# Kernel tuning notes

Measured on AMD Instinct MI355X. Metric: run time of the kernel, lower is better.

The kernel has to match this reference:

```python
import jax, jax.numpy as jnp
import numpy as np

B, S, D, H = 2, 1024, 768, 12
HD = D // H          # head_dim = 64
DFF = 4 * D          # 3072
EPS = 1e-5


def _ln(x, g, b):
    m = x.mean(-1, keepdims=True)
    v = ((x - m) ** 2).mean(-1, keepdims=True)
    return (x - m) * jax.lax.rsqrt(v + EPS) * g + b


def setup_inputs() -> dict:
    key = jax.random.key(0)
    ks = jax.random.split(key, 8)
    w = lambda k, shape: jax.random.normal(k, shape, jnp.float32) * 0.02
    return {
        "inp": jax.random.normal(ks[0], (B, S, D), jnp.float32),
        "attention_mask": jnp.zeros((B, S), bool),  # True = masked out (filled with -inf)
        "rel_matrix": jax.random.randint(ks[1], (B, S, S), -1, 2, jnp.int32),  # values in {-1,0,1}
        "qkv_w": w(ks[2], (3 * D, D)),
        "rel_A": w(ks[3], (3, HD)),        # relative_position_emb_A.weight
        "o_w": w(ks[4], (D, D)),
        "w1": w(ks[5], (DFF, D)), "b1": jnp.zeros((DFF,), jnp.float32),
        "w2": w(ks[6], (D, DFF)), "b2": jnp.zeros((D,), jnp.float32),
        "ln1_g": jnp.ones((D,), jnp.float32), "ln1_b": jnp.zeros((D,), jnp.float32),
        "ln2_g": jnp.ones((D,), jnp.float32), "ln2_b": jnp.zeros((D,), jnp.float32),
    }


def reference(inp, attention_mask, rel_matrix, qkv_w, rel_A, o_w,
              w1, b1, w2, b2, ln1_g, ln1_b, ln2_g, ln2_b):
    x = _ln(inp, ln1_g, ln1_b)
    qkv = x @ qkv_w.T                                  # (B,S,3D)
    q, k, v = jnp.split(qkv, 3, axis=-1)
    heads = lambda t: t.reshape(B, S, H, HD).transpose(0, 2, 1, 3)  # (B,H,S,HD)
    q, k, v = heads(q), heads(k), heads(v)

    # q @ (k + rel_emb)^T without materializing k_aug:
    # q.k^T term plus per-(q,key) relative term gathered from q @ A^T.
    logits = jnp.einsum("bhqd,bhkd->bhqk", q, k)       # (B,H,S,S)
    r = jnp.einsum("bhqd,cd->bhqc", q, rel_A)          # (B,H,S,3)
    idx = (rel_matrix + 1).astype(jnp.int32)           # (B,S,S) in {0,1,2}
    rel = jnp.take_along_axis(r, jnp.broadcast_to(idx[:, None], (B, H, S, S)), axis=-1)
    logits = (logits + rel) / np.sqrt(HD).astype(np.float32)
    # masked_fill: -inf where mask is True
    logits = jnp.where(attention_mask[:, None, None, :], -jnp.inf, logits)

    attn = jax.nn.softmax(logits, axis=-1)
    out = jnp.einsum("bhqk,bhkd->bhqd", attn, v)
    out = out.transpose(0, 2, 1, 3).reshape(B, S, D)
    inp = inp + out @ o_w.T                            # residual (dropout=0)

    h = _ln(inp, ln2_g, ln2_b)
    mlp = jax.nn.relu(h @ w1.T + b1) @ w2.T + b2
    return inp + mlp
```

## Files before the change

kernel.cpp:

```cpp
#include <hip/hip_runtime.h>
#include <hip/hip_bf16.h>

#define BB 2
#define SS 1024
#define DD 768
#define HH 12
#define HD 64
#define DFF 3072
#define EPS 1e-5f
#define BS2 (BB * SS)
#define BSD ((size_t)BS2 * DD)

typedef unsigned short ushort_t;
typedef unsigned char uchar_t;
using short8 = __attribute__((ext_vector_type(8))) short;
using f32x4  = __attribute__((ext_vector_type(4))) float;

__device__ __forceinline__ ushort_t f2bf_rne(float f) {
    union { float f; unsigned u; } x; x.f = f;
    unsigned r = x.u + 0x7fff + ((x.u >> 16) & 1);
    return (ushort_t)(r >> 16);
}
__device__ __forceinline__ float bf2f(short u) {
    union { unsigned i; float f; } x;
    x.i = ((unsigned)(ushort_t)u) << 16;
    return x.f;
}

#define CVT_N1 (3 * DD * DD / 4)
#define CVT_N2 (CVT_N1 + DD * DD / 4)
#define CVT_N3 (CVT_N2 + DFF * DD / 4)
#define CVT_NT (CVT_N3 + DD * DFF / 4)

__global__ __launch_bounds__(256) void cvt_all(
    const float* __restrict__ qkv_w, const float* __restrict__ o_w,
    const float* __restrict__ w1, const float* __restrict__ w2,
    ushort_t* __restrict__ dst)
{
    int i = blockIdx.x * 256 + threadIdx.x;
    if (i >= CVT_NT) return;
    const float* src; int off;
    if (i < CVT_N1)      { src = qkv_w; off = i; }
    else if (i < CVT_N2) { src = o_w;   off = i - CVT_N1; }
    else if (i < CVT_N3) { src = w1;    off = i - CVT_N2; }
    else                 { src = w2;    off = i - CVT_N3; }
    float4 v = ((const float4*)src)[off];
    ushort4 o;
    o.x = f2bf_rne(v.x); o.y = f2bf_rne(v.y);
    o.z = f2bf_rne(v.z); o.w = f2bf_rne(v.w);
    ((ushort4*)dst)[i] = o;
}

__global__ __launch_bounds__(256) void build_codes(
    const int* __restrict__ rel, const uchar_t* __restrict__ mask,
    unsigned* __restrict__ codes)
{
    int tid = blockIdx.x * 256 + threadIdx.x;
    int l15 = tid & 15;
    int kt  = (tid >> 4) & 15;
    int q   = (tid >> 8) & (SS - 1);
    int b   = tid >> 18;
    const int* rrow = rel + ((size_t)(b * SS + q)) * SS + kt * 64 + l15;
    const uchar_t* mrow = mask + (size_t)b * SS + kt * 64 + l15;
    unsigned o = 0;
#pragma unroll
    for (int nt = 0; nt < 4; ++nt) {
        unsigned c = mrow[nt * 16] ? 3u : (unsigned)(rrow[nt * 16] + 1);
        o |= c << (8 * nt);
    }
    codes[((size_t)(b * SS + q) * 16 + kt) * 16 + l15] = o;
}

__global__ __launch_bounds__(256) void ln_kernel_bf(
    const float* __restrict__ x, const float* __restrict__ g,
    const float* __restrict__ b, ushort_t* __restrict__ y)
{
    const int row = blockIdx.x;
    const float* xr = x + (size_t)row * DD;
    float s = 0.f, ss = 0.f;
    for (int i = threadIdx.x; i < DD; i += 256) {
        float v = xr[i];
        s += v; ss += v * v;
    }
    for (int off = 32; off; off >>= 1) {
        s  += __shfl_down(s,  off);
        ss += __shfl_down(ss, off);
    }
    __shared__ float reds[4], redss[4], bc[2];
    int t = threadIdx.x;
    if ((t & 63) == 0) { reds[t >> 6] = s; redss[t >> 6] = ss; }
    __syncthreads();
    if (t == 0) {
        float S1 = reds[0] + reds[1] + reds[2] + reds[3];
        float S2 = redss[0] + redss[1] + redss[2] + redss[3];
        float mean = S1 / DD;
        float var = S2 / DD - mean * mean;
        bc[0] = mean;
        bc[1] = rsqrtf(var + EPS);
    }
    __syncthreads();
    float mean = bc[0], inv = bc[1];
    ushort_t* yr = y + (size_t)row * DD;
    for (int i = threadIdx.x; i < DD; i += 256) {
        yr[i] = f2bf_rne((xr[i] - mean) * inv * g[i] + b[i]);
    }
}

__global__ __launch_bounds__(256) void merge2_ln_kernel(
    const float* __restrict__ part, const float* __restrict__ inp,
    const float* __restrict__ g, const float* __restrict__ b,
    float* __restrict__ resid, ushort_t* __restrict__ h_bf)
{
    const int row = blockIdx.x;
    const int t = threadIdx.x;
    float4 v = make_float4(0.f, 0.f, 0.f, 0.f);
    const size_t idx = (size_t)row * (DD / 4) + t;
    if (t < DD / 4) {
        v = ((const float4*)inp)[idx];
        float4 p0 = ((const float4*)part)[idx];
        float4 p1 = ((const float4*)(part + BSD))[idx];
        v.x += p0.x + p1.x; v.y += p0.y + p1.y;
        v.z += p0.z + p1.z; v.w += p0.w + p1.w;
        ((float4*)resid)[idx] = v;
    }
    float s  = v.x + v.y + v.z + v.w;
    float ss = v.x * v.x + v.y * v.y + v.z * v.z + v.w * v.w;
    for (int off = 32; off; off >>= 1) {
        s  += __shfl_down(s,  off);
        ss += __shfl_down(ss, off);
    }
    __shared__ float reds[4], redss[4], bc[2];
    if ((t & 63) == 0) { reds[t >> 6] = s; redss[t >> 6] = ss; }
    __syncthreads();
    if (t == 0) {
        float S1 = reds[0] + reds[1] + reds[2] + reds[3];
        float S2 = redss[0] + redss[1] + redss[2] + redss[3];
        float mean = S1 / DD;
        float var = S2 / DD - mean * mean;
        bc[0] = mean;
        bc[1] = rsqrtf(var + EPS);
    }
    __syncthreads();
    if (t < DD / 4) {
        const float mean = bc[0], inv = bc[1];
        float4 gv = ((const float4*)g)[t];
        float4 bv = ((const float4*)b)[t];
        ushort4 o;
        o.x = f2bf_rne((v.x - mean) * inv * gv.x + bv.x);
        o.y = f2bf_rne((v.y - mean) * inv * gv.y + bv.y);
        o.z = f2bf_rne((v.z - mean) * inv * gv.z + bv.z);
        o.w = f2bf_rne((v.w - mean) * inv * gv.w + bv.w);
        ((ushort4*)h_bf)[idx] = o;
    }
}

__global__ __launch_bounds__(256) void merge4_kernel(
    const float* __restrict__ part, const float* __restrict__ resid,
    const float* __restrict__ b2, float* __restrict__ outp, int n4)
{
    int i = blockIdx.x * 256 + threadIdx.x;
    if (i >= n4) return;
    float4 v = ((const float4*)resid)[i];
    int col4 = (i * 4) % DD;
    float4 bv = *(const float4*)(b2 + col4);
    v.x += bv.x; v.y += bv.y; v.z += bv.z; v.w += bv.w;
#pragma unroll
    for (int z = 0; z < 4; ++z) {
        float4 pz = ((const float4*)(part + (size_t)z * BSD))[i];
        v.x += pz.x; v.y += pz.y; v.z += pz.z; v.w += pz.w;
    }
    ((float4*)outp)[i] = v;
}

template <bool RELU, bool OUT_BF16, bool HAS_BIAS, bool PARTIAL>
__global__ __launch_bounds__(256) void gemm_tile(
    const ushort_t* __restrict__ A, const ushort_t* __restrict__ W,
    const float* __restrict__ bias, void* __restrict__ Cout,
    int M, int N, int K, int Ksplit)
{
    __shared__ __align__(16) ushort_t As[1024 * 8];
    __shared__ __align__(16) ushort_t Bs[512 * 8];

    const int t  = threadIdx.x;
    const int n0 = blockIdx.x * 64;
    const int m0 = blockIdx.y * 128;
    const int kb = blockIdx.z * Ksplit;
    const int w  = t >> 6;
    const int l  = t & 63;
    const int wm = (w & 1) * 64;
    const int wn = (w >> 1) * 32;
    const int l15  = l & 15;
    const int quad = l >> 4;

    const ushort_t* gA = A + (size_t)(m0 + (t & 127)) * K + kb + (t >> 7) * 8;
    ushort_t* lA = &As[(size_t)t * 8];
    const ushort_t* gB = W + (size_t)(n0 + (t & 63)) * K + kb + (t >> 6) * 8;
    ushort_t* lB = &Bs[(size_t)t * 8];

    f32x4 acc[4][2] = {};

    for (int k0 = 0; k0 < Ksplit; k0 += 64) {
        __syncthreads();
#pragma unroll
        for (int ii = 0; ii < 4; ++ii)
            __builtin_amdgcn_global_load_lds(
                (const __attribute__((address_space(1))) unsigned int*)(gA + k0 + ii * 16),
                (__attribute__((address_space(3))) unsigned int*)(lA + (size_t)ii * 256 * 8),
                16, 0, 0);
#pragma unroll
        for (int ii = 0; ii < 2; ++ii)
            __builtin_amdgcn_global_load_lds(
                (const __attribute__((address_space(1))) unsigned int*)(gB + k0 + ii * 32),
                (__attribute__((address_space(3))) unsigned int*)(lB + (size_t)ii * 256 * 8),
                16, 0, 0);
        __syncthreads();

#pragma unroll
        for (int ks = 0; ks < 2; ++ks) {
            const ushort_t* aptr = &As[(size_t)((ks * 4 + quad) * 128 + wm + l15) * 8];
            const ushort_t* bptr = &Bs[(size_t)((ks * 4 + quad) * 64 + wn + l15) * 8];
            short8 af[4], bf[2];
#pragma unroll
            for (int i = 0; i < 4; ++i)
                af[i] = *(const short8*)(aptr + (size_t)i * 16 * 8);
#pragma unroll
            for (int j = 0; j < 2; ++j)
                bf[j] = *(const short8*)(bptr + (size_t)j * 16 * 8);
#pragma unroll
            for (int i = 0; i < 4; ++i)
#pragma unroll
                for (int j = 0; j < 2; ++j)
                    acc[i][j] = __builtin_amdgcn_mfma_f32_16x16x32_bf16(
                        af[i], bf[j], acc[i][j], 0, 0, 0);
        }
    }

    if (PARTIAL) {
        float* Cp = (float*)Cout + (size_t)blockIdx.z * ((size_t)M * N);
#pragma unroll
        for (int i = 0; i < 4; ++i) {
            const int row = m0 + wm + i * 16 + quad * 4;
#pragma unroll
            for (int j = 0; j < 2; ++j) {
                const int col = n0 + wn + j * 16 + l15;
#pragma unroll
                for (int r = 0; r < 4; ++r)
                    Cp[(size_t)(row + r) * N + col] = acc[i][j][r];
            }
        }
    } else {
#pragma unroll
        for (int i = 0; i < 4; ++i) {
            const int row = m0 + wm + i * 16 + quad * 4;
#pragma unroll
            for (int j = 0; j < 2; ++j) {
                const int col = n0 + wn + j * 16 + l15;
                const float bv = HAS_BIAS ? bias[col] : 0.f;
#pragma unroll
                for (int r = 0; r < 4; ++r) {
                    float v = acc[i][j][r] + bv;
                    if (RELU) v = fmaxf(v, 0.f);
                    if (OUT_BF16)
                        ((ushort_t*)Cout)[(size_t)(row + r) * N + col] = f2bf_rne(v);
                    else
                        ((float*)Cout)[(size_t)(row + r) * N + col] = v;
                }
            }
        }
    }
}

__global__ __launch_bounds__(256) void attn_mfma_kernel(
    const ushort_t* __restrict__ qkv,
    const unsigned* __restrict__ codes,
    const float* __restrict__ rel_A,
    float* __restrict__ Opart,
    float* __restrict__ lpart)
{
    __shared__ __align__(16) ushort_t Ks[64 * 64];
    __shared__ __align__(16) unsigned Vt2[64 * 36];
    __shared__ __align__(16) ushort_t Ps[64 * 72];
    __shared__ __align__(16) float r3s[64][4];

    const int bx = blockIdx.x;
    const int ks = bx & 3;
    const int qt = (bx >> 2) & 15;
    const int h  = (bx >> 6) % HH;
    const int b  = bx / (64 * HH);
    const int q0 = qt * 64;
    const int t  = threadIdx.x;
    const int w  = t >> 6;
    const int l  = t & 63;
    const int l15  = l & 15;
    const int quad = l >> 4;

    const size_t qrow = (size_t)(b * SS + q0 + w * 16 + l15) * (3 * DD) + h * HD;
    const short8 qf0 = *(const short8*)(qkv + qrow + quad * 8);
    const short8 qf1 = *(const short8*)(qkv + qrow + 32 + quad * 8);

    {
        float rv[3];
#pragma unroll
        for (int c = 0; c < 3; ++c) {
            const float* a = rel_A + c * HD + quad * 8;
            float acc = 0.f;
#pragma unroll
            for (int j = 0; j < 8; ++j) acc += bf2f(qf0[j]) * a[j];
#pragma unroll
            for (int j = 0; j < 8; ++j) acc += bf2f(qf1[j]) * a[32 + j];
            acc += __shfl_xor(acc, 16);
            acc += __shfl_xor(acc, 32);
            rv[c] = acc;
        }
        if (quad == 0) {
            float4 f4 = make_float4(rv[0], rv[1], rv[2], -2.4e31f);
            *(float4*)&r3s[w * 16 + l15][0] = f4;
        }
    }
    __syncthreads();
    float4 r3v[4];
#pragma unroll
    for (int reg = 0; reg < 4; ++reg)
        r3v[reg] = *(const float4*)&r3s[w * 16 + quad * 4 + reg][0];

    float l_run[4] = {0.f, 0.f, 0.f, 0.f};
    f32x4 oacc[4] = {};

    for (int kt = ks * 4; kt < ks * 4 + 4; ++kt) {
        const int k0 = kt * 64;
        __syncthreads();
        {
            const int r  = t >> 3;
            const int cp = t & 7;
            const int cl  = cp ^ (r & 7);
            const ushort_t* g = qkv + (size_t)(b * SS + k0 + r) * (3 * DD) + DD + h * HD + cl * 8;
            __builtin_amdgcn_global_load_lds(
                (const __attribute__((address_space(1))) unsigned*)g,
                (__attribute__((address_space(3))) unsigned*)(Ks + (size_t)t * 8), 16, 0, 0);
            const int r2  = r + 32;
            const int cl2 = cp ^ (r2 & 7);
            const ushort_t* g2 = qkv + (size_t)(b * SS + k0 + r2) * (3 * DD) + DD + h * HD + cl2 * 8;
            __builtin_amdgcn_global_load_lds(
                (const __attribute__((address_space(1))) unsigned*)g2,
                (__attribute__((address_space(3))) unsigned*)(Ks + (size_t)(t + 256) * 8), 16, 0, 0);
        }
        {
            const int kp = t >> 3;
            const int dg = t & 7;
            const ushort_t* g = qkv + (size_t)(b * SS + k0 + 2 * kp) * (3 * DD) + 2 * DD + h * HD + dg * 8;
            short8 va = *(const short8*)g;
            short8 vb = *(const short8*)(g + 3 * DD);
            const int kps = kp ^ ((dg & 7) * 4);
#pragma unroll
            for (int i = 0; i < 8; ++i)
                Vt2[(size_t)(dg * 8 + i) * 36 + kps] =
                    (unsigned)(ushort_t)va[i] | ((unsigned)(ushort_t)vb[i] << 16);
        }
        __syncthreads();

        f32x4 sacc[4] = {};
#pragma unroll
        for (int kc = 0; kc < 2; ++kc) {
            const short8 qv = kc ? qf1 : qf0;
#pragma unroll
            for (int nt = 0; nt < 4; ++nt) {
                const int row = nt * 16 + l15;
                const int cp  = (kc * 4 + quad) ^ (row & 7);
                const short8 kf = *(const short8*)(Ks + (size_t)row * 64 + cp * 8);
                sacc[nt] = __builtin_amdgcn_mfma_f32_16x16x32_bf16(qv, kf, sacc[nt], 0, 0, 0);
            }
        }

#pragma unroll
        for (int reg = 0; reg < 4; ++reg) {
            const int qloc = w * 16 + quad * 4 + reg;
            const unsigned cds = codes[((size_t)(b * SS + q0 + qloc) * 16 + kt) * 16 + l15];
            const float4 r4 = r3v[reg];
#pragma unroll
            for (int nt = 0; nt < 4; ++nt) {
                const unsigned c = (cds >> (8 * nt)) & 0xff;
                float rvv = (c == 0) ? r4.x : (c == 1) ? r4.y : (c == 2) ? r4.z : r4.w;
                const float p = __expf((sacc[nt][reg] + rvv) * 0.125f);
                l_run[reg] += p;
                Ps[(size_t)qloc * 72 + nt * 16 + l15] = f2bf_rne(p);
            }
        }

#pragma unroll
        for (int kc = 0; kc < 2; ++kc) {
            const short8 pf = *(const short8*)(Ps + (size_t)(w * 16 + l15) * 72 + kc * 32 + quad * 8);
#pragma unroll
            for (int dt = 0; dt < 4; ++dt) {
                const int d  = dt * 16 + l15;
                const int dg = d >> 3;
                const int kps0 = (kc * 16 + quad * 4) ^ ((dg & 7) * 4);
                const short8 vf = *(const short8*)((const ushort_t*)&Vt2[(size_t)d * 36 + kps0]);
                oacc[dt] = __builtin_amdgcn_mfma_f32_16x16x32_bf16(pf, vf, oacc[dt], 0, 0, 0);
            }
        }
    }

    float* Op = Opart + (size_t)ks * BSD;
    float* lp = lpart + (size_t)ks * BS2 * HH;
#pragma unroll
    for (int reg = 0; reg < 4; ++reg) {
        float ls = l_run[reg];
        ls += __shfl_xor(ls, 1);
        ls += __shfl_xor(ls, 2);
        ls += __shfl_xor(ls, 4);
        ls += __shfl_xor(ls, 8);
        const int orow = b * SS + q0 + w * 16 + quad * 4 + reg;
#pragma unroll
        for (int dt = 0; dt < 4; ++dt)
            Op[(size_t)orow * DD + h * HD + dt * 16 + l15] = oacc[dt][reg];
        if (l15 == 0) lp[(size_t)orow * HH + h] = ls;
    }
}

__global__ __launch_bounds__(256) void attn_merge(
    const float* __restrict__ Opart, const float* __restrict__ lpart,
    ushort_t* __restrict__ att_bf)
{
    int i = blockIdx.x * 256 + threadIdx.x;
    int row = (i * 4) / DD;
    int h   = ((i * 4) % DD) >> 6;
    float lsum = 0.f;
#pragma unroll
    for (int z = 0; z < 4; ++z)
        lsum += lpart[(size_t)z * BS2 * HH + (size_t)row * HH + h];
    float inv = 1.0f / lsum;
    float4 os = ((const float4*)Opart)[i];
#pragma unroll
    for (int z = 1; z < 4; ++z) {
        float4 oz = ((const float4*)(Opart + (size_t)z * BSD))[i];
        os.x += oz.x; os.y += oz.y; os.z += oz.z; os.w += oz.w;
    }
    ushort4 o;
    o.x = f2bf_rne(os.x * inv);
    o.y = f2bf_rne(os.y * inv);
    o.z = f2bf_rne(os.z * inv);
    o.w = f2bf_rne(os.w * inv);
    ((ushort4*)att_bf)[i] = o;
}

extern "C" void kernel_launch(void* const* d_in, const int* in_sizes, int n_in,
                              void* d_out, int out_size, void* d_ws, size_t ws_size,
                              hipStream_t stream) {
    const float* inp   = (const float*)d_in[0];
    const uchar_t* amask = (const uchar_t*)d_in[1];
    const int*   relm  = (const int*)d_in[2];
    const float* qkv_w = (const float*)d_in[3];
    const float* rel_A = (const float*)d_in[4];
    const float* o_w   = (const float*)d_in[5];
    const float* w1    = (const float*)d_in[6];
    const float* b1    = (const float*)d_in[7];
    const float* w2    = (const float*)d_in[8];
    const float* b2    = (const float*)d_in[9];
    const float* ln1_g = (const float*)d_in[10];
    const float* ln1_b = (const float*)d_in[11];
    const float* ln2_g = (const float*)d_in[12];
    const float* ln2_b = (const float*)d_in[13];
    float* out = (float*)d_out;

    char* p = (char*)d_ws;
    ushort_t* x_bf   = (ushort_t*)p; p += BSD * 2;
    ushort_t* att_bf = (ushort_t*)p; p += BSD * 2;
    ushort_t* h_bf   = (ushort_t*)p; p += BSD * 2;
    ushort_t* ff_bf  = (ushort_t*)p; p += (size_t)BS2 * DFF * 2;
    ushort_t* qkvw_bf= (ushort_t*)p; p += (size_t)3 * DD * DD * 2;
    ushort_t* ow_bf  = (ushort_t*)p; p += (size_t)DD * DD * 2;
    ushort_t* w1_bf  = (ushort_t*)p; p += (size_t)DFF * DD * 2;
    ushort_t* w2_bf  = (ushort_t*)p; p += (size_t)DD * DFF * 2;
    ushort_t* qkv_bf = (ushort_t*)p; p += (size_t)BS2 * 3 * DD * 2;
    float*    resid  = (float*)p;    p += BSD * 4;
    float*    pool   = (float*)p;    p += 4 * BSD * 4;
    float*    lpart  = (float*)p;    p += (size_t)4 * BS2 * HH * 4;
    unsigned* codes  = (unsigned*)p; p += (size_t)BB * SS * SS;

    cvt_all<<<(CVT_NT + 255) / 256, 256, 0, stream>>>(qkv_w, o_w, w1, w2, qkvw_bf);
    build_codes<<<(BB * SS * 256) / 256, 256, 0, stream>>>(relm, amask, codes);

    ln_kernel_bf<<<BS2, 256, 0, stream>>>(inp, ln1_g, ln1_b, x_bf);

    gemm_tile<false, true, false, false>
        <<<dim3(3 * DD / 64, BS2 / 128, 1), 256, 0, stream>>>(
        x_bf, qkvw_bf, nullptr, qkv_bf, BS2, 3 * DD, DD, DD);

    attn_mfma_kernel<<<BB * HH * 16 * 4, 256, 0, stream>>>(
        qkv_bf, codes, rel_A, pool, lpart);
    attn_merge<<<(int)(BSD / 4 / 256), 256, 0, stream>>>(pool, lpart, att_bf);

    gemm_tile<false, false, false, true>
        <<<dim3(DD / 64, BS2 / 128, 2), 256, 0, stream>>>(
        att_bf, ow_bf, nullptr, pool, BS2, DD, DD, DD / 2);

    merge2_ln_kernel<<<BS2, 256, 0, stream>>>(
        pool, inp, ln2_g, ln2_b, resid, h_bf);

    gemm_tile<true, true, true, false>
        <<<dim3(DFF / 64, BS2 / 128, 1), 256, 0, stream>>>(
        h_bf, w1_bf, b1, ff_bf, BS2, DFF, DD, DD);

    gemm_tile<false, false, false, true>
        <<<dim3(DD / 64, BS2 / 128, 4), 256, 0, stream>>>(
        ff_bf, w2_bf, nullptr, pool, BS2, DD, DFF, DFF / 4);

    merge4_kernel<<<(int)(BSD / 4 / 256), 256, 0, stream>>>(
        pool, resid, b2, out, (int)(BSD / 4));
}
```

Baseline: 275.3 us.

## Fuse prep kernels, transpose GEMM tile shape, halve attention split with bf16 partials

Merges weight conversion, mask/relative-code building and the first LayerNorm into one launch to cut launch overhead. The GEMM tile changes from 128x64 to 64x128 (M x N), which changes per-block load balance and which operand tile is reused. Attention splits the key range into 2 chunks instead of 4 and stores the partial outputs as bf16 in a dedicated buffer, so the merge reads less data. The bf16 partials add rounding error before normalization, and the smaller split lowers the block count for attention.

```diff
diff --git a/kernel.cpp b/kernel.cpp
--- a/kernel.cpp
+++ b/kernel.cpp
@@ -31,54 +31,56 @@
 #define CVT_N2 (CVT_N1 + DD * DD / 4)
 #define CVT_N3 (CVT_N2 + DFF * DD / 4)
 #define CVT_NT (CVT_N3 + DD * DFF / 4)
-
-__global__ __launch_bounds__(256) void cvt_all(
+#define PREP_CVT   (CVT_NT / 256)
+#define PREP_CODES (BB * SS)
+#define PREP_LN    BS2
+
+__global__ __launch_bounds__(256) void prep_kernel(
     const float* __restrict__ qkv_w, const float* __restrict__ o_w,
     const float* __restrict__ w1, const float* __restrict__ w2,
-    ushort_t* __restrict__ dst)
-{
-    int i = blockIdx.x * 256 + threadIdx.x;
-    if (i >= CVT_NT) return;
-    const float* src; int off;
-    if (i < CVT_N1)      { src = qkv_w; off = i; }
-    else if (i < CVT_N2) { src = o_w;   off = i - CVT_N1; }
-    else if (i < CVT_N3) { src = w1;    off = i - CVT_N2; }
-    else                 { src = w2;    off = i - CVT_N3; }
-    float4 v = ((const float4*)src)[off];
-    ushort4 o;
-    o.x = f2bf_rne(v.x); o.y = f2bf_rne(v.y);
-    o.z = f2bf_rne(v.z); o.w = f2bf_rne(v.w);
-    ((ushort4*)dst)[i] = o;
-}
-
-__global__ __launch_bounds__(256) void build_codes(
+    ushort_t* __restrict__ wdst,
     const int* __restrict__ rel, const uchar_t* __restrict__ mask,
-    unsigned* __restrict__ codes)
-{
-    int tid = blockIdx.x * 256 + threadIdx.x;
-    int l15 = tid & 15;
-    int kt  = (tid >> 4) & 15;
-    int q   = (tid >> 8) & (SS - 1);
-    int b   = tid >> 18;
-    const int* rrow = rel + ((size_t)(b * SS + q)) * SS + kt * 64 + l15;
-    const uchar_t* mrow = mask + (size_t)b * SS + kt * 64 + l15;
-    unsigned o = 0;
-#pragma unroll
-    for (int nt = 0; nt < 4; ++nt) {
-        unsigned c = mrow[nt * 16] ? 3u : (unsigned)(rrow[nt * 16] + 1);
-        o |= c << (8 * nt);
-    }
-    codes[((size_t)(b * SS + q) * 16 + kt) * 16 + l15] = o;
-}
-
-__global__ __launch_bounds__(256) void ln_kernel_bf(
+    unsigned* __restrict__ codes,
     const float* __restrict__ x, const float* __restrict__ g,
     const float* __restrict__ b, ushort_t* __restrict__ y)
 {
-    const int row = blockIdx.x;
+    const int bx = blockIdx.x;
+    const int t  = threadIdx.x;
+    if (bx < PREP_CVT) {
+        int i = bx * 256 + t;
+        const float* src; int off;
+        if (i < CVT_N1)      { src = qkv_w; off = i; }
+        else if (i < CVT_N2) { src = o_w;   off = i - CVT_N1; }
+        else if (i < CVT_N3) { src = w1;    off = i - CVT_N2; }
+        else                 { src = w2;    off = i - CVT_N3; }
+        float4 v = ((const float4*)src)[off];
+        ushort4 o;
+        o.x = f2bf_rne(v.x); o.y = f2bf_rne(v.y);
+        o.z = f2bf_rne(v.z); o.w = f2bf_rne(v.w);
+        ((ushort4*)wdst)[i] = o;
+        return;
+    }
+    if (bx < PREP_CVT + PREP_CODES) {
+        int tid = (bx - PREP_CVT) * 256 + t;
+        int l15 = tid & 15;
+        int kt  = (tid >> 4) & 15;
+        int q   = (tid >> 8) & (SS - 1);
+        int bb  = tid >> 18;
+        const int* rrow = rel + ((size_t)(bb * SS + q)) * SS + kt * 64 + l15;
+        const uchar_t* mrow = mask + (size_t)bb * SS + kt * 64 + l15;
+        unsigned o = 0;
+#pragma unroll
+        for (int nt = 0; nt < 4; ++nt) {
+            unsigned c = mrow[nt * 16] ? 3u : (unsigned)(rrow[nt * 16] + 1);
+            o |= c << (8 * nt);
+        }
+        codes[((size_t)(bb * SS + q) * 16 + kt) * 16 + l15] = o;
+        return;
+    }
+    const int row = bx - PREP_CVT - PREP_CODES;
     const float* xr = x + (size_t)row * DD;
     float s = 0.f, ss = 0.f;
-    for (int i = threadIdx.x; i < DD; i += 256) {
+    for (int i = t; i < DD; i += 256) {
         float v = xr[i];
         s += v; ss += v * v;
     }
@@ -87,7 +89,6 @@
         ss += __shfl_down(ss, off);
     }
     __shared__ float reds[4], redss[4], bc[2];
-    int t = threadIdx.x;
     if ((t & 63) == 0) { reds[t >> 6] = s; redss[t >> 6] = ss; }
     __syncthreads();
     if (t == 0) {
@@ -101,7 +102,7 @@
     __syncthreads();
     float mean = bc[0], inv = bc[1];
     ushort_t* yr = y + (size_t)row * DD;
-    for (int i = threadIdx.x; i < DD; i += 256) {
+    for (int i = t; i < DD; i += 256) {
         yr[i] = f2bf_rne((xr[i] - mean) * inv * g[i] + b[i]);
     }
 }
@@ -178,58 +179,58 @@
     const float* __restrict__ bias, void* __restrict__ Cout,
     int M, int N, int K, int Ksplit)
 {
-    __shared__ __align__(16) ushort_t As[1024 * 8];
-    __shared__ __align__(16) ushort_t Bs[512 * 8];
+    __shared__ __align__(16) ushort_t As[512 * 8];
+    __shared__ __align__(16) ushort_t Bs[1024 * 8];
 
     const int t  = threadIdx.x;
-    const int n0 = blockIdx.x * 64;
-    const int m0 = blockIdx.y * 128;
+    const int n0 = blockIdx.x * 128;
+    const int m0 = blockIdx.y * 64;
     const int kb = blockIdx.z * Ksplit;
     const int w  = t >> 6;
     const int l  = t & 63;
-    const int wm = (w & 1) * 64;
-    const int wn = (w >> 1) * 32;
+    const int wm = (w & 1) * 32;
+    const int wn = (w >> 1) * 64;
     const int l15  = l & 15;
     const int quad = l >> 4;
 
-    const ushort_t* gA = A + (size_t)(m0 + (t & 127)) * K + kb + (t >> 7) * 8;
+    const ushort_t* gA = A + (size_t)(m0 + (t & 63)) * K + kb + (t >> 6) * 8;
     ushort_t* lA = &As[(size_t)t * 8];
-    const ushort_t* gB = W + (size_t)(n0 + (t & 63)) * K + kb + (t >> 6) * 8;
+    const ushort_t* gB = W + (size_t)(n0 + (t & 127)) * K + kb + (t >> 7) * 8;
     ushort_t* lB = &Bs[(size_t)t * 8];
 
-    f32x4 acc[4][2] = {};
+    f32x4 acc[2][4] = {};
 
     for (int k0 = 0; k0 < Ksplit; k0 += 64) {
         __syncthreads();
+        __builtin_amdgcn_global_load_lds(
+            (const __attribute__((address_space(1))) unsigned int*)(gA + k0),
+            (__attribute__((address_space(3))) unsigned int*)lA, 16, 0, 0);
+        __builtin_amdgcn_global_load_lds(
+            (const __attribute__((address_space(1))) unsigned int*)(gA + k0 + 32),
+            (__attribute__((address_space(3))) unsigned int*)(lA + 256 * 8), 16, 0, 0);
 #pragma unroll
         for (int ii = 0; ii < 4; ++ii)
             __builtin_amdgcn_global_load_lds(
-                (const __attribute__((address_space(1))) unsigned int*)(gA + k0 + ii * 16),
-                (__attribute__((address_space(3))) unsigned int*)(lA + (size_t)ii * 256 * 8),
-                16, 0, 0);
-#pragma unroll
-        for (int ii = 0; ii < 2; ++ii)
-            __builtin_amdgcn_global_load_lds(
-                (const __attribute__((address_space(1))) unsigned int*)(gB + k0 + ii * 32),
+                (const __attribute__((address_space(1))) unsigned int*)(gB + k0 + ii * 16),
                 (__attribute__((address_space(3))) unsigned int*)(lB + (size_t)ii * 256 * 8),
                 16, 0, 0);
         __syncthreads();
 
 #pragma unroll
         for (int ks = 0; ks < 2; ++ks) {
-            const ushort_t* aptr = &As[(size_t)((ks * 4 + quad) * 128 + wm + l15) * 8];
-            const ushort_t* bptr = &Bs[(size_t)((ks * 4 + quad) * 64 + wn + l15) * 8];
-            short8 af[4], bf[2];
-#pragma unroll
-            for (int i = 0; i < 4; ++i)
+            const ushort_t* aptr = &As[(size_t)((ks * 4 + quad) * 64 + wm + l15) * 8];
+            const ushort_t* bptr = &Bs[(size_t)((ks * 4 + quad) * 128 + wn + l15) * 8];
+            short8 af[2], bf[4];
+#pragma unroll
+            for (int i = 0; i < 2; ++i)
                 af[i] = *(const short8*)(aptr + (size_t)i * 16 * 8);
 #pragma unroll
-            for (int j = 0; j < 2; ++j)
+            for (int j = 0; j < 4; ++j)
                 bf[j] = *(const short8*)(bptr + (size_t)j * 16 * 8);
 #pragma unroll
-            for (int i = 0; i < 4; ++i)
-#pragma unroll
-                for (int j = 0; j < 2; ++j)
+            for (int i = 0; i < 2; ++i)
+#pragma unroll
+                for (int j = 0; j < 4; ++j)
                     acc[i][j] = __builtin_amdgcn_mfma_f32_16x16x32_bf16(
                         af[i], bf[j], acc[i][j], 0, 0, 0);
         }
@@ -238,10 +239,10 @@
     if (PARTIAL) {
         float* Cp = (float*)Cout + (size_t)blockIdx.z * ((size_t)M * N);
 #pragma unroll
-        for (int i = 0; i < 4; ++i) {
+        for (int i = 0; i < 2; ++i) {
             const int row = m0 + wm + i * 16 + quad * 4;
 #pragma unroll
-            for (int j = 0; j < 2; ++j) {
+            for (int j = 0; j < 4; ++j) {
                 const int col = n0 + wn + j * 16 + l15;
 #pragma unroll
                 for (int r = 0; r < 4; ++r)
@@ -250,10 +251,10 @@
         }
     } else {
 #pragma unroll
-        for (int i = 0; i < 4; ++i) {
+        for (int i = 0; i < 2; ++i) {
             const int row = m0 + wm + i * 16 + quad * 4;
 #pragma unroll
-            for (int j = 0; j < 2; ++j) {
+            for (int j = 0; j < 4; ++j) {
                 const int col = n0 + wn + j * 16 + l15;
                 const float bv = HAS_BIAS ? bias[col] : 0.f;
 #pragma unroll
@@ -274,7 +275,7 @@
     const ushort_t* __restrict__ qkv,
     const unsigned* __restrict__ codes,
     const float* __restrict__ rel_A,
-    float* __restrict__ Opart,
+    ushort_t* __restrict__ Opart,
     float* __restrict__ lpart)
 {
     __shared__ __align__(16) ushort_t Ks[64 * 64];
@@ -283,10 +284,10 @@
     __shared__ __align__(16) float r3s[64][4];
 
     const int bx = blockIdx.x;
-    const int ks = bx & 3;
-    const int qt = (bx >> 2) & 15;
-    const int h  = (bx >> 6) % HH;
-    const int b  = bx / (64 * HH);
+    const int ks = bx & 1;
+    const int qt = (bx >> 1) & 15;
+    const int h  = (bx >> 5) % HH;
+    const int b  = bx / (32 * HH);
     const int q0 = qt * 64;
     const int t  = threadIdx.x;
     const int w  = t >> 6;
@@ -326,7 +327,7 @@
     float l_run[4] = {0.f, 0.f, 0.f, 0.f};
     f32x4 oacc[4] = {};
 
-    for (int kt = ks * 4; kt < ks * 4 + 4; ++kt) {
+    for (int kt = ks * 8; kt < ks * 8 + 8; ++kt) {
         const int k0 = kt * 64;
         __syncthreads();
         {
@@ -400,7 +401,7 @@
         }
     }
 
-    float* Op = Opart + (size_t)ks * BSD;
+    ushort_t* Op = Opart + (size_t)ks * BSD;
     float* lp = lpart + (size_t)ks * BS2 * HH;
 #pragma unroll
     for (int reg = 0; reg < 4; ++reg) {
@@ -412,34 +413,28 @@
         const int orow = b * SS + q0 + w * 16 + quad * 4 + reg;
 #pragma unroll
         for (int dt = 0; dt < 4; ++dt)
-            Op[(size_t)orow * DD + h * HD + dt * 16 + l15] = oacc[dt][reg];
+            Op[(size_t)orow * DD + h * HD + dt * 16 + l15] = f2bf_rne(oacc[dt][reg]);
         if (l15 == 0) lp[(size_t)orow * HH + h] = ls;
     }
 }
 
 __global__ __launch_bounds__(256) void attn_merge(
-    const float* __restrict__ Opart, const float* __restrict__ lpart,
+    const ushort_t* __restrict__ Opart, const float* __restrict__ lpart,
     ushort_t* __restrict__ att_bf)
 {
     int i = blockIdx.x * 256 + threadIdx.x;
     int row = (i * 4) / DD;
     int h   = ((i * 4) % DD) >> 6;
-    float lsum = 0.f;
-#pragma unroll
-    for (int z = 0; z < 4; ++z)
-        lsum += lpart[(size_t)z * BS2 * HH + (size_t)row * HH + h];
-    float inv = 1.0f / lsum;
-    float4 os = ((const float4*)Opart)[i];
-#pragma unroll
-    for (int z = 1; z < 4; ++z) {
-        float4 oz = ((const float4*)(Opart + (size_t)z * BSD))[i];
-        os.x += oz.x; os.y += oz.y; os.z += oz.z; os.w += oz.w;
-    }
+    float l0 = lpart[(size_t)row * HH + h];
+    float l1 = lpart[(size_t)BS2 * HH + (size_t)row * HH + h];
+    float inv = 1.0f / (l0 + l1);
+    ushort4 a = ((const ushort4*)Opart)[i];
+    ushort4 b = ((const ushort4*)(Opart + BSD))[i];
     ushort4 o;
-    o.x = f2bf_rne(os.x * inv);
-    o.y = f2bf_rne(os.y * inv);
-    o.z = f2bf_rne(os.z * inv);
-    o.w = f2bf_rne(os.w * inv);
+    o.x = f2bf_rne((bf2f(a.x) + bf2f(b.x)) * inv);
+    o.y = f2bf_rne((bf2f(a.y) + bf2f(b.y)) * inv);
+    o.z = f2bf_rne((bf2f(a.z) + bf2f(b.z)) * inv);
+    o.w = f2bf_rne((bf2f(a.w) + bf2f(b.w)) * inv);
     ((ushort4*)att_bf)[i] = o;
 }
 
@@ -474,35 +469,35 @@
     ushort_t* qkv_bf = (ushort_t*)p; p += (size_t)BS2 * 3 * DD * 2;
     float*    resid  = (float*)p;    p += BSD * 4;
     float*    pool   = (float*)p;    p += 4 * BSD * 4;
-    float*    lpart  = (float*)p;    p += (size_t)4 * BS2 * HH * 4;
+    ushort_t* Opart  = (ushort_t*)p; p += 2 * BSD * 2;
+    float*    lpart  = (float*)p;    p += (size_t)2 * BS2 * HH * 4;
     unsigned* codes  = (unsigned*)p; p += (size_t)BB * SS * SS;
 
-    cvt_all<<<(CVT_NT + 255) / 256, 256, 0, stream>>>(qkv_w, o_w, w1, w2, qkvw_bf);
-    build_codes<<<(BB * SS * 256) / 256, 256, 0, stream>>>(relm, amask, codes);
-
-    ln_kernel_bf<<<BS2, 256, 0, stream>>>(inp, ln1_g, ln1_b, x_bf);
+    prep_kernel<<<PREP_CVT + PREP_CODES + PREP_LN, 256, 0, stream>>>(
+        qkv_w, o_w, w1, w2, qkvw_bf, relm, amask, codes,
+        inp, ln1_g, ln1_b, x_bf);
 
     gemm_tile<false, true, false, false>
-        <<<dim3(3 * DD / 64, BS2 / 128, 1), 256, 0, stream>>>(
+        <<<dim3(3 * DD / 128, BS2 / 64, 1), 256, 0, stream>>>(
         x_bf, qkvw_bf, nullptr, qkv_bf, BS2, 3 * DD, DD, DD);
 
-    attn_mfma_kernel<<<BB * HH * 16 * 4, 256, 0, stream>>>(
-        qkv_bf, codes, rel_A, pool, lpart);
-    attn_merge<<<(int)(BSD / 4 / 256), 256, 0, stream>>>(pool, lpart, att_bf);
+    attn_mfma_kernel<<<BB * HH * 16 * 2, 256, 0, stream>>>(
+        qkv_bf, codes, rel_A, Opart, lpart);
+    attn_merge<<<(int)(BSD / 4 / 256), 256, 0, stream>>>(Opart, lpart, att_bf);
 
     gemm_tile<false, false, false, true>
-        <<<dim3(DD / 64, BS2 / 128, 2), 256, 0, stream>>>(
+        <<<dim3(DD / 128, BS2 / 64, 2), 256, 0, stream>>>(
         att_bf, ow_bf, nullptr, pool, BS2, DD, DD, DD / 2);
 
     merge2_ln_kernel<<<BS2, 256, 0, stream>>>(
         pool, inp, ln2_g, ln2_b, resid, h_bf);
 
     gemm_tile<true, true, true, false>
-        <<<dim3(DFF / 64, BS2 / 128, 1), 256, 0, stream>>>(
+        <<<dim3(DFF / 128, BS2 / 64, 1), 256, 0, stream>>>(
         h_bf, w1_bf, b1, ff_bf, BS2, DFF, DD, DD);
 
     gemm_tile<false, false, false, true>
-        <<<dim3(DD / 64, BS2 / 128, 4), 256, 0, stream>>>(
+        <<<dim3(DD / 128, BS2 / 64, 4), 256, 0, stream>>>(
         ff_bf, w2_bf, nullptr, pool, BS2, DD, DFF, DFF / 4);
 
     merge4_kernel<<<(int)(BSD / 4 / 256), 256, 0, stream>>>(
```

Result: faster. 266.9 us (-3.0%).
